# Optimization experiments

Measured on AMD Instinct MI355X. Metric: run time of the kernel, lower is better.

The kernel has to match this reference:

```python
import jax, jax.numpy as jnp
import numpy as np

B, N, IN, H, I, A, NA, NH = 4096, 8, 256, 256, 64, 64, 32, 256
VAR_FLOOR = 0.002
BN_EPS = 1e-5


def _lin(x, w, b):
    # torch Linear: x @ w.T + b, w: [out, in]
    return x @ w.T + b


def _bn_train(x, g, b):
    # BatchNorm1d in training mode: batch stats, biased variance
    mu = jnp.mean(x, axis=0)
    var = jnp.var(x, axis=0)
    return (x - mu) * jax.lax.rsqrt(var + BN_EPS) * g + b


def _intent_net(h_la, w1, b1, g, bbn, w2, b2):
    z = _lin(h_la, w1, b1)
    z = _bn_train(z, g, bbn)
    z = jax.nn.leaky_relu(z, 0.01)
    return _lin(z, w2, b2)


def setup_inputs() -> dict:
    key = jax.random.key(0)
    ks = jax.random.split(key, 30)
    s = 0.05
    d = {
        "inputs": jax.random.normal(ks[0], (B * N, IN), jnp.float32),
        "last_actions": jax.random.normal(ks[1], (B, N, NA), jnp.float32),
        "hidden_state": jax.random.normal(ks[2], (B * N, H), jnp.float32),
        "eps": jax.random.normal(ks[3], (B * N, I), jnp.float32),
        # fc1
        "fc1_w": jax.random.normal(ks[4], (H, IN), jnp.float32) * s,
        "fc1_b": jnp.zeros((H,), jnp.float32),
        # GRUCell (r,z,n gate order, torch layout)
        "gru_w_ih": jax.random.normal(ks[5], (3 * H, H), jnp.float32) * s,
        "gru_w_hh": jax.random.normal(ks[6], (3 * H, H), jnp.float32) * s,
        "gru_b_ih": jnp.zeros((3 * H,), jnp.float32),
        "gru_b_hh": jnp.zeros((3 * H,), jnp.float32),
        # intent_net: Linear(H+NA, NH) -> BN -> LeakyReLU -> Linear(NH, 2*I)
        "in1_w": jax.random.normal(ks[7], (NH, H + NA), jnp.float32) * s,
        "in1_b": jnp.zeros((NH,), jnp.float32),
        "bn_g": jnp.ones((NH,), jnp.float32),
        "bn_b": jnp.zeros((NH,), jnp.float32),
        "in2_w": jax.random.normal(ks[8], (2 * I, NH), jnp.float32) * s,
        "in2_b": jnp.zeros((2 * I,), jnp.float32),
        # attention projections
        "wq_w": jax.random.normal(ks[9], (A, I), jnp.float32) * s,
        "wq_b": jnp.zeros((A,), jnp.float32),
        "wk_w": jax.random.normal(ks[10], (A, I), jnp.float32) * s,
        "wk_b": jnp.zeros((A,), jnp.float32),
        "wv_w": jax.random.normal(ks[11], (A, I + H), jnp.float32) * s,
        "wv_b": jnp.zeros((A,), jnp.float32),
        # fc2
        "fc2_w": jax.random.normal(ks[12], (NA, H + A), jnp.float32) * s,
        "fc2_b": jnp.zeros((NA,), jnp.float32),
        "bs": B,
        "t": 1,
    }
    return d


def reference(inputs, last_actions, hidden_state, eps,
              fc1_w, fc1_b, gru_w_ih, gru_w_hh, gru_b_ih, gru_b_hh,
              in1_w, in1_b, bn_g, bn_b, in2_w, in2_b,
              wq_w, wq_b, wk_w, wk_b, wv_w, wv_b, fc2_w, fc2_b,
              bs, t):
    n = N
    x = jax.nn.relu(_lin(inputs, fc1_w, fc1_b))  # [bs*n, H]
    h_in = hidden_state.reshape(-1, H)
    # torch GRUCell
    gi = x @ gru_w_ih.T + gru_b_ih
    gh = h_in @ gru_w_hh.T + gru_b_hh
    i_r, i_z, i_n = jnp.split(gi, 3, axis=-1)
    h_r, h_z, h_n = jnp.split(gh, 3, axis=-1)
    r = jax.nn.sigmoid(i_r + h_r)
    z = jax.nn.sigmoid(i_z + h_z)
    nng = jnp.tanh(i_n + r * h_n)
    h = (1.0 - z) * nng + z * h_in  # [bs*n, H]

    la = last_actions.reshape(bs * n, NA)
    h_la = jnp.concatenate([h, la], axis=-1)
    ip = _intent_net(h_la, in1_w, in1_b, bn_g, bn_b, in2_w, in2_b)  # [bs*n, 2I]
    mean = ip[:, :I]
    std = jnp.maximum(jnp.exp(ip[:, I:]), VAR_FLOOR)
    intent = mean + eps * std  # reparameterized sample, [bs*n, I]

    q = _lin(intent, wq_w, wq_b).reshape(bs, n, A)  # query per agent i
    k = _lin(intent, wk_w, wk_b).reshape(bs, n, A)  # key per agent j
    scale = 1.0 / jnp.sqrt(jnp.float32(A))
    alpha = jnp.einsum('bia,bja->bij', q * scale, k)  # [bs, n, n]
    diag = jnp.eye(n, dtype=bool)
    alpha = jnp.where(diag[None], -1e9, alpha)
    alpha = jax.nn.softmax(alpha, axis=-1)

    v = _lin(jnp.concatenate([intent, h], axis=-1), wv_w, wv_b).reshape(bs, n, A)
    combined = jnp.einsum('bij,bja->bia', alpha, v).reshape(bs * n, A)

    local_Q = _lin(jnp.concatenate([h, combined], axis=-1), fc2_w, fc2_b).reshape(bs, n, NA)
    # final intent_embed: fresh intent_net output (no clamp/exp applied)
    intent_embed = _intent_net(h_la, in1_w, in1_b, bn_g, bn_b, in2_w, in2_b)
    return local_Q, h, intent, intent_embed
```

## Files before the change

### kernel.cpp

```cpp
#include <hip/hip_runtime.h>
#include <hip/hip_bf16.h>

#define BN_ 32768

using bf16 = __hip_bfloat16;
typedef __bf16 v8bf __attribute__((ext_vector_type(8)));
typedef unsigned short v8us __attribute__((ext_vector_type(8)));
typedef float v4f __attribute__((ext_vector_type(4)));

__device__ __forceinline__ float b2f(bf16 x) { return __bfloat162float(x); }
__device__ __forceinline__ bf16 f2b(float x) { return __float2bfloat16(x); }
__device__ __forceinline__ unsigned short f2bu(float x) {
  bf16 h = __float2bfloat16(x);
  return *reinterpret_cast<unsigned short*>(&h);
}
__device__ __forceinline__ float bu2f(unsigned short u) {
  union { unsigned int i; float f; } x;
  x.i = ((unsigned int)u) << 16;
  return x.f;
}
__device__ __forceinline__ void gl_lds16(const void* g, void* l) {
  __builtin_amdgcn_global_load_lds(
      (const __attribute__((address_space(1))) void*)g,
      (__attribute__((address_space(3))) void*)l, 16, 0, 0);
}
__device__ __forceinline__ float fsig(float x) { return 1.f / (1.f + __expf(-x)); }
__device__ __forceinline__ float ftanh(float x) {
  return 1.f - 2.f / (__expf(2.f * x) + 1.f);
}
template <int CF>
__device__ __forceinline__ void cstore(void* C, size_t off, float v) {
  if constexpr (CF) ((float*)C)[off] = v;
  else ((bf16*)C)[off] = f2b(v);
}
__device__ __forceinline__ int xcd_swz() {
  const int nbx = gridDim.x, nby = gridDim.y;
  const int f = blockIdx.y * nbx + blockIdx.x;
  const int nwg = nbx * nby;
  const int q = nwg >> 3, r = nwg & 7;
  const int xcd = f & 7, l = f >> 3;
  if (r == 0) return xcd * q + l;
  return (xcd < r ? xcd * (q + 1) : r * (q + 1) + (xcd - r) * q) + l;
}

template <int TM, int TN, int WR, int WC, int ACT, int A1M, int A2M, int KS, int KSB,
          int CF>
__global__ __launch_bounds__(256) void gemm_bt(
    const void* __restrict__ A1, int lda1, const void* __restrict__ A2, int lda2,
    const bf16* __restrict__ B1, const bf16* __restrict__ B2, int ldb,
    const float* __restrict__ bias, void* C, int ldc, int K) {
  constexpr int BK = 64;
  __shared__ __align__(16) unsigned short As[TM * BK];
  __shared__ __align__(16) unsigned short Bs[TN * BK];
  const int tid = threadIdx.x;
  const int wv = tid >> 6;
  const int lane = tid & 63;
  const int w = xcd_swz();
  const int bm = (w / gridDim.y) * TM;
  const int bn = (w % gridDim.y) * TN;

  constexpr int WM = TM / WR, WN = TN / WC;
  constexpr int FM = WM / 16, FN = WN / 16;
  const int wm0 = (wv % WR) * WM;
  const int wn0 = (wv / WR) * WN;

  v4f acc[FM][FN];
  const v4f vzero = {0.f, 0.f, 0.f, 0.f};
  for (int i = 0; i < FM; ++i)
    for (int j = 0; j < FN; ++j) acc[i][j] = vzero;

  const int lrow = lane >> 3;
  const int lcol = (lane & 7) * 8;
  const int mr = lane & 15;
  const int kq = (lane >> 4) * 8;

  for (int k0 = 0; k0 < K; k0 += BK) {
    {
      const bool useA1 = (KS == 0) || (k0 < KS);
      const void* Ap = useA1 ? A1 : A2;
      const int lda = useA1 ? lda1 : lda2;
      const int ka = useA1 ? k0 : k0 - KS;
      const bool f32 = useA1 ? (A1M == 1) : (A2M == 1);
      if (f32) {
        const float* Af = (const float*)Ap;
        for (int ch = wv; ch < TM / 8; ch += 4) {
          const float* s = Af + (size_t)(bm + ch * 8 + lrow) * lda + ka + lcol;
          float4 x0 = *(const float4*)s;
          float4 x1 = *(const float4*)(s + 4);
          v8us d;
          d[0]=f2bu(x0.x); d[1]=f2bu(x0.y); d[2]=f2bu(x0.z); d[3]=f2bu(x0.w);
          d[4]=f2bu(x1.x); d[5]=f2bu(x1.y); d[6]=f2bu(x1.z); d[7]=f2bu(x1.w);
          *(v8us*)(As + ch * 8 * BK + lane * 8) = d;
        }
      } else {
        const unsigned short* Ab = (const unsigned short*)Ap;
        for (int ch = wv; ch < TM / 8; ch += 4)
          gl_lds16(Ab + (size_t)(bm + ch * 8 + lrow) * lda + ka + lcol,
                   As + ch * 8 * BK);
      }
    }
    {
      const bool useB1 = (KSB == 0) || (k0 < KSB);
      const bf16* Bp = useB1 ? B1 : B2;
      const int kb = useB1 ? k0 : k0 - KSB;
      for (int ch = wv; ch < TN / 8; ch += 4)
        gl_lds16((const unsigned short*)Bp + (size_t)(bn + ch * 8 + lrow) * ldb + kb + lcol,
                 Bs + ch * 8 * BK);
    }
    __syncthreads();
#pragma unroll
    for (int kk = 0; kk < BK; kk += 32) {
      v8bf af[FM], bfr[FN];
#pragma unroll
      for (int i = 0; i < FM; ++i)
        af[i] = *(const v8bf*)(As + (wm0 + i * 16 + mr) * BK + kk + kq);
#pragma unroll
      for (int j = 0; j < FN; ++j)
        bfr[j] = *(const v8bf*)(Bs + (wn0 + j * 16 + mr) * BK + kk + kq);
#pragma unroll
      for (int i = 0; i < FM; ++i)
#pragma unroll
        for (int j = 0; j < FN; ++j)
          acc[i][j] = __builtin_amdgcn_mfma_f32_16x16x32_bf16(af[i], bfr[j],
                                                              acc[i][j], 0, 0, 0);
    }
    __syncthreads();
  }
  const int crow = (lane >> 4) * 4;
#pragma unroll
  for (int j = 0; j < FN; ++j) {
    const int gcol = bn + wn0 + j * 16 + mr;
    const float bv = bias[gcol];
#pragma unroll
    for (int i = 0; i < FM; ++i) {
#pragma unroll
      for (int r = 0; r < 4; ++r) {
        const int grow = bm + wm0 + i * 16 + crow + r;
        size_t off = (size_t)grow * ldc + gcol;
        float v = acc[i][j][r] + bv;
        if (ACT == 1) v = v > 0.f ? v : 0.f;
        cstore<CF>(C, off, v);
      }
    }
  }
}

__global__ __launch_bounds__(256) void gru_fused(
    const bf16* __restrict__ X, const bf16* __restrict__ HB,
    const bf16* __restrict__ Win, const bf16* __restrict__ Whn,
    const float* __restrict__ FBp, const bf16* __restrict__ G1,
    float* __restrict__ Hout) {
  constexpr int BK = 64;
  __shared__ __align__(16) char smem[69632];
  unsigned short* AsX = (unsigned short*)smem;
  unsigned short* AsH = AsX + 8192;
  unsigned short* Bin = AsH + 8192;
  unsigned short* Bhn = Bin + 8192;
  float* Ein = (float*)smem;
  float* Ehn = (float*)(smem + 34816);

  const int tid = threadIdx.x;
  const int wv = tid >> 6;
  const int lane = tid & 63;
  const int w = xcd_swz();
  const int bm = (w / gridDim.y) * 128;
  const int bn = (w % gridDim.y) * 128;
  const int wm0 = (wv & 1) * 64;
  const int wn0 = (wv >> 1) * 64;

  v4f ain[4][4], ahn[4][4];
  const v4f vzero = {0.f, 0.f, 0.f, 0.f};
  for (int i = 0; i < 4; ++i)
    for (int j = 0; j < 4; ++j) { ain[i][j] = vzero; ahn[i][j] = vzero; }

  const int lrow = lane >> 3;
  const int lcol = (lane & 7) * 8;
  const int mr = lane & 15;
  const int kq = (lane >> 4) * 8;

  for (int k0 = 0; k0 < 256; k0 += BK) {
    for (int ch = wv; ch < 16; ch += 4) {
      const size_t aoff = (size_t)(bm + ch * 8 + lrow) * 256 + k0 + lcol;
      gl_lds16((const unsigned short*)X + aoff, AsX + ch * 8 * BK);
      gl_lds16((const unsigned short*)HB + aoff, AsH + ch * 8 * BK);
      const size_t boff = (size_t)(bn + ch * 8 + lrow) * 256 + k0 + lcol;
      gl_lds16((const unsigned short*)Win + boff, Bin + ch * 8 * BK);
      gl_lds16((const unsigned short*)Whn + boff, Bhn + ch * 8 * BK);
    }
    __syncthreads();
#pragma unroll
    for (int kk = 0; kk < BK; kk += 32) {
      v8bf ax[4], ah[4], bi[4], bh[4];
#pragma unroll
      for (int i = 0; i < 4; ++i) {
        ax[i] = *(const v8bf*)(AsX + (wm0 + i * 16 + mr) * BK + kk + kq);
        ah[i] = *(const v8bf*)(AsH + (wm0 + i * 16 + mr) * BK + kk + kq);
      }
#pragma unroll
      for (int j = 0; j < 4; ++j) {
        bi[j] = *(const v8bf*)(Bin + (wn0 + j * 16 + mr) * BK + kk + kq);
        bh[j] = *(const v8bf*)(Bhn + (wn0 + j * 16 + mr) * BK + kk + kq);
      }
#pragma unroll
      for (int i = 0; i < 4; ++i)
#pragma unroll
        for (int j = 0; j < 4; ++j) {
          ain[i][j] = __builtin_amdgcn_mfma_f32_16x16x32_bf16(ax[i], bi[j],
                                                              ain[i][j], 0, 0, 0);
          ahn[i][j] = __builtin_amdgcn_mfma_f32_16x16x32_bf16(ah[i], bh[j],
                                                              ahn[i][j], 0, 0, 0);
        }
    }
    __syncthreads();
  }

  const int crow = (lane >> 4) * 4;
  const int myhalf = wn0 >> 6;
  const int c4 = (tid & 15) * 4;
#pragma unroll
  for (int h = 0; h < 2; ++h) {
    __syncthreads();
    if (myhalf == h) {
#pragma unroll
      for (int i = 0; i < 4; ++i)
#pragma unroll
        for (int j = 0; j < 4; ++j)
#pragma unroll
          for (int r = 0; r < 4; ++r) {
            const int idx = (wm0 + i * 16 + crow + r) * 68 + j * 16 + mr;
            Ein[idx] = ain[i][j][r];
            Ehn[idx] = ahn[i][j][r];
          }
    }
    __syncthreads();
#pragma unroll
    for (int it = 0; it < 8; ++it) {
      const int row = (tid >> 4) + it * 16;
      const int grow = bm + row;
      const int gcol = bn + h * 64 + c4;
      const unsigned short* g1p = (const unsigned short*)G1 + (size_t)grow * 512 + gcol;
      const ushort4 r4 = *(const ushort4*)g1p;
      const ushort4 z4 = *(const ushort4*)(g1p + 256);
      const ushort4 hp4 = *(const ushort4*)((const unsigned short*)HB +
                                            (size_t)grow * 256 + gcol);
      const float4 ei = *(const float4*)(Ein + row * 68 + c4);
      const float4 eh = *(const float4*)(Ehn + row * 68 + c4);
      const float4 bin4 = *(const float4*)(FBp + 768 + gcol);
      const float4 bhn4 = *(const float4*)(FBp + 1024 + gcol);
      const float rv[4] = {bu2f(r4.x), bu2f(r4.y), bu2f(r4.z), bu2f(r4.w)};
      const float zv[4] = {bu2f(z4.x), bu2f(z4.y), bu2f(z4.z), bu2f(z4.w)};
      const float hpv[4] = {bu2f(hp4.x), bu2f(hp4.y), bu2f(hp4.z), bu2f(hp4.w)};
      const float eiv[4] = {ei.x, ei.y, ei.z, ei.w};
      const float ehv[4] = {eh.x, eh.y, eh.z, eh.w};
      const float biv[4] = {bin4.x, bin4.y, bin4.z, bin4.w};
      const float bhv[4] = {bhn4.x, bhn4.y, bhn4.z, bhn4.w};
      float vo[4];
#pragma unroll
      for (int u = 0; u < 4; ++u) {
        float rr = fsig(rv[u]);
        float zz = fsig(zv[u]);
        float nn = ftanh(eiv[u] + biv[u] + rr * (ehv[u] + bhv[u]));
        vo[u] = (1.f - zz) * nn + zz * hpv[u];
      }
      *(float4*)(Hout + (size_t)grow * 256 + gcol) =
          make_float4(vo[0], vo[1], vo[2], vo[3]);
    }
  }
}

__global__ void conv_all(
    const float* fc1_w, const float* w_ih, const float* w_hh, const float* in1_w,
    const float* in2_w, const float* wq_w, const float* wk_w, const float* wv_w,
    const float* fc2_w, const float* fc1_b, const float* b_ih, const float* b_hh,
    const float* in1_b, const float* in2_b, const float* wq_b, const float* wk_b,
    const float* wv_b, const float* fc2_b, const float* bn_g, const float* bn_b,
    bf16* __restrict__ WF, float* __restrict__ FB) {
  int idx = blockIdx.x * 256 + threadIdx.x;
  if (idx < 612352) {
    float v;
    if (idx < 65536) v = fc1_w[idx];
    else if (idx < 262144) v = w_ih[idx - 65536];
    else if (idx < 458752) v = w_hh[idx - 262144];
    else if (idx < 540672) {
      int j = idx - 458752, r = j / 320, c = j % 320;
      v = (c < 288) ? in1_w[r * 288 + c] : 0.f;
    } else if (idx < 573440) v = in2_w[idx - 540672];
    else if (idx < 581632) {
      int j = idx - 573440, r = j >> 6, c = j & 63;
      v = (r < 64) ? wq_w[r * 64 + c] : wk_w[(r - 64) * 64 + c];
    } else if (idx < 602112) v = wv_w[idx - 581632];
    else v = fc2_w[idx - 602112];
    WF[idx] = f2b(v);
  } else if (idx < 615936) {
    int j = idx - 612352;
    float v;
    if (j < 256) v = fc1_b[j];
    else if (j < 768) v = b_ih[j - 256] + b_hh[j - 256];
    else if (j < 1024) v = b_ih[512 + j - 768];
    else if (j < 1280) v = b_hh[512 + j - 1024];
    else if (j < 1536) v = in1_b[j - 1280];
    else if (j < 1664) v = in2_b[j - 1536];
    else if (j < 1792) { int c = j - 1664; v = (c < 64) ? wq_b[c] : wk_b[c - 64]; }
    else if (j < 1856) v = wv_b[j - 1792];
    else if (j < 1888) v = fc2_b[j - 1856];
    else if (j < 2144) v = bn_g[j - 1888];
    else if (j < 2400) v = bn_b[j - 2144];
    else v = 0.f;
    FB[j] = v;
  }
}

__global__ void f2b_copy(const float* __restrict__ s, bf16* __restrict__ d) {
  int i = blockIdx.x * 256 + threadIdx.x;
  const float4 a = ((const float4*)s)[i * 2];
  const float4 b = ((const float4*)s)[i * 2 + 1];
  v8us o;
  o[0]=f2bu(a.x); o[1]=f2bu(a.y); o[2]=f2bu(a.z); o[3]=f2bu(a.w);
  o[4]=f2bu(b.x); o[5]=f2bu(b.y); o[6]=f2bu(b.z); o[7]=f2bu(b.w);
  ((v8us*)d)[i] = o;
}

__global__ void pack_la(const float* __restrict__ la, bf16* __restrict__ lap) {
  int idx = blockIdx.x * 256 + threadIdx.x;
  int row = idx >> 6, c = idx & 63;
  lap[idx] = f2b((c < 32) ? la[(size_t)row * 32 + c] : 0.f);
}

__global__ void bn_reduce(const bf16* __restrict__ Z1, float* __restrict__ stats) {
  int col = threadIdx.x;
  float s = 0.f, q = 0.f;
  for (int r = blockIdx.x; r < BN_; r += 256) {
    float v = b2f(Z1[(size_t)r * 256 + col]);
    s += v; q += v * v;
  }
  atomicAdd(&stats[col], s);
  atomicAdd(&stats[256 + col], q);
}

__global__ void bn_finalize(const float* __restrict__ g, const float* __restrict__ b,
                            float* __restrict__ stats) {
  int c = threadIdx.x;
  float mean = stats[c] * (1.f / 32768.f);
  float var = stats[256 + c] * (1.f / 32768.f) - mean * mean;
  var = fmaxf(var, 0.f);
  float sc = g[c] * rsqrtf(var + 1e-5f);
  stats[512 + c] = sc;
  stats[768 + c] = b[c] - mean * sc;
}

__global__ void bn_leaky(const bf16* __restrict__ Z1, const float* __restrict__ stats,
                         bf16* __restrict__ zt) {
  int idx = blockIdx.x * 256 + threadIdx.x;
  int col = idx & 255;
  float v = b2f(Z1[idx]) * stats[512 + col] + stats[768 + col];
  zt[idx] = f2b(v > 0.f ? v : 0.01f * v);
}

__global__ void make_intent(const float* __restrict__ ie, const float* __restrict__ eps,
                            float* __restrict__ intent) {
  int idx = blockIdx.x * 256 + threadIdx.x;
  int row = idx >> 6, c = idx & 63;
  float mean = ie[(size_t)row * 128 + c];
  float sd = fmaxf(expf(ie[(size_t)row * 128 + 64 + c]), 0.002f);
  intent[idx] = mean + eps[idx] * sd;
}

__global__ __launch_bounds__(64) void attn(const bf16* __restrict__ QK,
                                           const bf16* __restrict__ Vv,
                                           bf16* __restrict__ comb) {
  __shared__ float q[8][65], k[8][65], v[8][65];
  __shared__ float al[8][8];
  int b = blockIdx.x, t = threadIdx.x;
  size_t rb = (size_t)b * 8;
  for (int u = 0; u < 8; ++u) {
    q[u][t] = b2f(QK[(rb + u) * 128 + t]);
    k[u][t] = b2f(QK[(rb + u) * 128 + 64 + t]);
    v[u][t] = b2f(Vv[(rb + u) * 64 + t]);
  }
  __syncthreads();
  int i = t >> 3, j = t & 7;
  float s = 0.f;
#pragma unroll
  for (int a = 0; a < 64; ++a) s += q[i][a] * k[j][a];
  s *= 0.125f;
  if (i == j) s = -1e9f;
  float m = s;
  m = fmaxf(m, __shfl_xor(m, 1, 8));
  m = fmaxf(m, __shfl_xor(m, 2, 8));
  m = fmaxf(m, __shfl_xor(m, 4, 8));
  float e = expf(s - m);
  float sum = e;
  sum += __shfl_xor(sum, 1, 8);
  sum += __shfl_xor(sum, 2, 8);
  sum += __shfl_xor(sum, 4, 8);
  al[i][j] = e / sum;
  __syncthreads();
  int a0 = (t & 7) * 8;
  for (int u = 0; u < 8; ++u) {
    float o = 0.f;
#pragma unroll
    for (int jj = 0; jj < 8; ++jj) o += al[i][jj] * v[jj][a0 + u];
    comb[(rb + i) * 64 + a0 + u] = f2b(o);
  }
}

extern "C" void kernel_launch(void* const* d_in, const int* in_sizes, int n_in,
                              void* d_out, int out_size, void* d_ws, size_t ws_size,
                              hipStream_t stream) {
  (void)in_sizes; (void)n_in; (void)out_size; (void)ws_size;
  const float* inputs = (const float*)d_in[0];
  const float* last_actions = (const float*)d_in[1];
  const float* hidden = (const float*)d_in[2];
  const float* eps = (const float*)d_in[3];

  float* out = (float*)d_out;
  float* out_lq = out;
  float* out_h = out + 1048576;
  float* out_it = out + 9437184;
  float* out_ie = out + 11534336;

  bf16* HB = (bf16*)(out + 11534336);

  char* ws = (char*)d_ws;
  bf16* X    = (bf16*)(ws + 0);
  bf16* G1   = (bf16*)(ws + 16777216);
  bf16* LAP  = (bf16*)(ws + 16777216);
  bf16* ZT   = (bf16*)(ws + 20971520);
  bf16* Z1   = (bf16*)(ws + 0);
  bf16* QK   = (bf16*)(ws + 0);
  bf16* V    = (bf16*)(ws + 8388608);
  bf16* COMB = (bf16*)(ws + 12582912);
  float* FB  = (float*)(ws + 50331648);
  bf16*  WF  = (bf16*)(ws + 50348032);
  float* stats = FB + 2560;

  conv_all<<<2406, 256, 0, stream>>>(
      (const float*)d_in[4], (const float*)d_in[6], (const float*)d_in[7],
      (const float*)d_in[10], (const float*)d_in[14], (const float*)d_in[16],
      (const float*)d_in[18], (const float*)d_in[20], (const float*)d_in[22],
      (const float*)d_in[5], (const float*)d_in[8], (const float*)d_in[9],
      (const float*)d_in[11], (const float*)d_in[15], (const float*)d_in[17],
      (const float*)d_in[19], (const float*)d_in[21], (const float*)d_in[23],
      (const float*)d_in[12], (const float*)d_in[13], WF, FB);

  f2b_copy<<<4096, 256, 0, stream>>>(hidden, HB);

  gemm_bt<128, 128, 2, 2, 1, 1, 0, 0, 0, 0><<<dim3(256, 2), 256, 0, stream>>>(
      inputs, 256, nullptr, 0, WF + 0, nullptr, 256, FB + 0, X, 256, 256);
  gemm_bt<128, 128, 2, 2, 0, 0, 0, 256, 256, 0><<<dim3(256, 4), 256, 0, stream>>>(
      X, 256, HB, 256, WF + 65536, WF + 262144, 256, FB + 256, G1, 512, 512);
  gru_fused<<<dim3(256, 2), 256, 0, stream>>>(
      X, HB, WF + 65536 + 512 * 256, WF + 262144 + 512 * 256, FB, G1, out_h);

  pack_la<<<8192, 256, 0, stream>>>(last_actions, LAP);
  gemm_bt<128, 128, 2, 2, 0, 1, 0, 256, 0, 0><<<dim3(256, 2), 256, 0, stream>>>(
      out_h, 256, LAP, 64, WF + 458752, nullptr, 320, FB + 1280, Z1, 256, 320);
  bn_reduce<<<256, 256, 0, stream>>>(Z1, stats);
  bn_finalize<<<1, 256, 0, stream>>>(FB + 1888, FB + 2144, stats);
  bn_leaky<<<32768, 256, 0, stream>>>(Z1, stats, ZT);
  gemm_bt<128, 128, 2, 2, 0, 0, 0, 0, 0, 1><<<dim3(256, 1), 256, 0, stream>>>(
      ZT, 256, nullptr, 0, WF + 540672, nullptr, 256, FB + 1536, out_ie, 128, 256);
  make_intent<<<8192, 256, 0, stream>>>(out_ie, eps, out_it);
  gemm_bt<128, 128, 2, 2, 0, 1, 0, 0, 0, 0><<<dim3(256, 1), 256, 0, stream>>>(
      out_it, 64, nullptr, 0, WF + 573440, nullptr, 64, FB + 1664, QK, 128, 64);
  gemm_bt<128, 64, 4, 1, 0, 1, 1, 64, 0, 0><<<dim3(256, 1), 256, 0, stream>>>(
      out_it, 64, out_h, 256, WF + 581632, nullptr, 320, FB + 1792, V, 64, 320);
  attn<<<4096, 64, 0, stream>>>(QK, V, COMB);
  gemm_bt<128, 32, 4, 1, 0, 1, 0, 256, 0, 1><<<dim3(256, 1), 256, 0, stream>>>(
      out_h, 256, COMB, 64, WF + 602112, nullptr, 320, FB + 1856, out_lq, 32, 320);
}
```

Measured before the change: 373.6 us.

## Fuse BN-apply into GEMM A-load, emit bf16 h/intent copies, vectorize BN and attention

The BN scale/shift and LeakyReLU are folded into the A-tile load of the second intent GEMM, which removes the separate bn_leaky pass and the ZT buffer. The GRU and make_intent kernels now also write bf16 copies of h and intent into a shared strided buffer, so later GEMMs read bf16 through the async LDS path instead of converting fp32 on every load. bn_reduce is vectorized with shared-memory partial reduction, and attn packs four batches per 256-thread block with vector loads and stores. LAP is moved into the output local_Q region, and the shared buffers are aliased in the workspace, which adds more extra writes and more aliasing risk.

After: 396.8 us. 1.06x slower.

```diff
diff --git a/kernel.cpp b/kernel.cpp
--- a/kernel.cpp
+++ b/kernel.cpp
@@ -44,11 +44,12 @@
 }
 
 template <int TM, int TN, int WR, int WC, int ACT, int A1M, int A2M, int KS, int KSB,
-          int CF>
+          int CF, int ATF>
 __global__ __launch_bounds__(256) void gemm_bt(
     const void* __restrict__ A1, int lda1, const void* __restrict__ A2, int lda2,
     const bf16* __restrict__ B1, const bf16* __restrict__ B2, int ldb,
-    const float* __restrict__ bias, void* C, int ldc, int K) {
+    const float* __restrict__ bias, void* C, int ldc, int K,
+    const float* __restrict__ tsc, const float* __restrict__ tsh) {
   constexpr int BK = 64;
   __shared__ __align__(16) unsigned short As[TM * BK];
   __shared__ __align__(16) unsigned short Bs[TN * BK];
@@ -81,7 +82,26 @@
       const int lda = useA1 ? lda1 : lda2;
       const int ka = useA1 ? k0 : k0 - KS;
       const bool f32 = useA1 ? (A1M == 1) : (A2M == 1);
-      if (f32) {
+      if (ATF && useA1) {
+        const unsigned short* Ab = (const unsigned short*)Ap;
+        const float4 s0 = *(const float4*)(tsc + ka + lcol);
+        const float4 s1 = *(const float4*)(tsc + ka + lcol + 4);
+        const float4 h0 = *(const float4*)(tsh + ka + lcol);
+        const float4 h1 = *(const float4*)(tsh + ka + lcol + 4);
+        const float sc[8] = {s0.x, s0.y, s0.z, s0.w, s1.x, s1.y, s1.z, s1.w};
+        const float sh[8] = {h0.x, h0.y, h0.z, h0.w, h1.x, h1.y, h1.z, h1.w};
+        for (int ch = wv; ch < TM / 8; ch += 4) {
+          const unsigned short* s = Ab + (size_t)(bm + ch * 8 + lrow) * lda + ka + lcol;
+          v8us zin = *(const v8us*)s;
+          v8us d;
+#pragma unroll
+          for (int u = 0; u < 8; ++u) {
+            float v = bu2f(zin[u]) * sc[u] + sh[u];
+            d[u] = f2bu(v > 0.f ? v : 0.01f * v);
+          }
+          *(v8us*)(As + ch * 8 * BK + lane * 8) = d;
+        }
+      } else if (f32) {
         const float* Af = (const float*)Ap;
         for (int ch = wv; ch < TM / 8; ch += 4) {
           const float* s = Af + (size_t)(bm + ch * 8 + lrow) * lda + ka + lcol;
@@ -148,7 +168,7 @@
 __global__ __launch_bounds__(256) void gru_fused(
     const bf16* __restrict__ X, const bf16* __restrict__ HB,
     const bf16* __restrict__ Win, const bf16* __restrict__ Whn,
-    const float* __restrict__ FBp, const bf16* __restrict__ G1,
+    const float* __restrict__ FBp, const bf16* G1, unsigned short* HB2,
     float* __restrict__ Hout) {
   constexpr int BK = 64;
   __shared__ __align__(16) char smem[69632];
@@ -264,6 +284,10 @@
       }
       *(float4*)(Hout + (size_t)grow * 256 + gcol) =
           make_float4(vo[0], vo[1], vo[2], vo[3]);
+      ushort4 hb2;
+      hb2.x = f2bu(vo[0]); hb2.y = f2bu(vo[1]);
+      hb2.z = f2bu(vo[2]); hb2.w = f2bu(vo[3]);
+      *(ushort4*)(HB2 + (size_t)grow * 512 + gcol) = hb2;
     }
   }
 }
@@ -326,15 +350,47 @@
   lap[idx] = f2b((c < 32) ? la[(size_t)row * 32 + c] : 0.f);
 }
 
-__global__ void bn_reduce(const bf16* __restrict__ Z1, float* __restrict__ stats) {
-  int col = threadIdx.x;
-  float s = 0.f, q = 0.f;
-  for (int r = blockIdx.x; r < BN_; r += 256) {
-    float v = b2f(Z1[(size_t)r * 256 + col]);
-    s += v; q += v * v;
-  }
-  atomicAdd(&stats[col], s);
-  atomicAdd(&stats[256 + col], q);
+__global__ __launch_bounds__(256) void bn_reduce(const bf16* __restrict__ Z1,
+                                                 float* __restrict__ stats) {
+  const int cg = threadIdx.x & 31;
+  const int rl = threadIdx.x >> 5;
+  float s[8], q[8];
+#pragma unroll
+  for (int u = 0; u < 8; ++u) { s[u] = 0.f; q[u] = 0.f; }
+  for (int r = blockIdx.x * 8 + rl; r < BN_; r += 2048) {
+    v8us z = *(const v8us*)((const unsigned short*)Z1 + (size_t)r * 256 + cg * 8);
+#pragma unroll
+    for (int u = 0; u < 8; ++u) {
+      float v = bu2f(z[u]);
+      s[u] += v; q[u] += v * v;
+    }
+  }
+  __shared__ float red[2048];
+#pragma unroll
+  for (int u = 0; u < 8; ++u) red[rl * 256 + cg * 8 + u] = s[u];
+  __syncthreads();
+  if (rl == 0) {
+#pragma unroll
+    for (int u = 0; u < 8; ++u) {
+      float t = 0.f;
+#pragma unroll
+      for (int k = 0; k < 8; ++k) t += red[k * 256 + cg * 8 + u];
+      atomicAdd(&stats[cg * 8 + u], t);
+    }
+  }
+  __syncthreads();
+#pragma unroll
+  for (int u = 0; u < 8; ++u) red[rl * 256 + cg * 8 + u] = q[u];
+  __syncthreads();
+  if (rl == 0) {
+#pragma unroll
+    for (int u = 0; u < 8; ++u) {
+      float t = 0.f;
+#pragma unroll
+      for (int k = 0; k < 8; ++k) t += red[k * 256 + cg * 8 + u];
+      atomicAdd(&stats[256 + cg * 8 + u], t);
+    }
+  }
 }
 
 __global__ void bn_finalize(const float* __restrict__ g, const float* __restrict__ b,
@@ -348,60 +404,74 @@
   stats[768 + c] = b[c] - mean * sc;
 }
 
-__global__ void bn_leaky(const bf16* __restrict__ Z1, const float* __restrict__ stats,
-                         bf16* __restrict__ zt) {
-  int idx = blockIdx.x * 256 + threadIdx.x;
-  int col = idx & 255;
-  float v = b2f(Z1[idx]) * stats[512 + col] + stats[768 + col];
-  zt[idx] = f2b(v > 0.f ? v : 0.01f * v);
-}
-
 __global__ void make_intent(const float* __restrict__ ie, const float* __restrict__ eps,
-                            float* __restrict__ intent) {
+                            float* __restrict__ intent, unsigned short* __restrict__ itb) {
   int idx = blockIdx.x * 256 + threadIdx.x;
   int row = idx >> 6, c = idx & 63;
   float mean = ie[(size_t)row * 128 + c];
   float sd = fmaxf(expf(ie[(size_t)row * 128 + 64 + c]), 0.002f);
-  intent[idx] = mean + eps[idx] * sd;
-}
-
-__global__ __launch_bounds__(64) void attn(const bf16* __restrict__ QK,
-                                           const bf16* __restrict__ Vv,
-                                           bf16* __restrict__ comb) {
-  __shared__ float q[8][65], k[8][65], v[8][65];
-  __shared__ float al[8][8];
-  int b = blockIdx.x, t = threadIdx.x;
-  size_t rb = (size_t)b * 8;
-  for (int u = 0; u < 8; ++u) {
-    q[u][t] = b2f(QK[(rb + u) * 128 + t]);
-    k[u][t] = b2f(QK[(rb + u) * 128 + 64 + t]);
-    v[u][t] = b2f(Vv[(rb + u) * 64 + t]);
+  float v = mean + eps[idx] * sd;
+  intent[idx] = v;
+  itb[(size_t)row * 512 + c] = f2bu(v);
+}
+
+__global__ __launch_bounds__(256) void attn(const bf16* __restrict__ QK,
+                                            const bf16* __restrict__ Vv,
+                                            bf16* __restrict__ comb) {
+  __shared__ float q[4][8][65], k[4][8][65], v[4][8][65];
+  __shared__ float al[4][8][8];
+  const int wv = threadIdx.x >> 6, t = threadIdx.x & 63;
+  const int b = blockIdx.x * 4 + wv;
+  const size_t rb = (size_t)b * 8;
+  const unsigned short* qkb = (const unsigned short*)QK + rb * 128;
+#pragma unroll
+  for (int p = 0; p < 2; ++p) {
+    const int e = t * 8 + p * 512;
+    const int row = e >> 7, col = e & 127;
+    v8us d = *(const v8us*)(qkb + row * 128 + col);
+    if (col < 64) {
+#pragma unroll
+      for (int u = 0; u < 8; ++u) q[wv][row][col + u] = bu2f(d[u]);
+    } else {
+#pragma unroll
+      for (int u = 0; u < 8; ++u) k[wv][row][col - 64 + u] = bu2f(d[u]);
+    }
+  }
+  {
+    const int e = t * 8;
+    const int row = e >> 6, col = e & 63;
+    v8us d = *(const v8us*)((const unsigned short*)Vv + rb * 64 + row * 64 + col);
+#pragma unroll
+    for (int u = 0; u < 8; ++u) v[wv][row][col + u] = bu2f(d[u]);
   }
   __syncthreads();
-  int i = t >> 3, j = t & 7;
+  const int i = t >> 3, j = t & 7;
   float s = 0.f;
 #pragma unroll
-  for (int a = 0; a < 64; ++a) s += q[i][a] * k[j][a];
+  for (int a = 0; a < 64; ++a) s += q[wv][i][a] * k[wv][j][a];
   s *= 0.125f;
   if (i == j) s = -1e9f;
   float m = s;
   m = fmaxf(m, __shfl_xor(m, 1, 8));
   m = fmaxf(m, __shfl_xor(m, 2, 8));
   m = fmaxf(m, __shfl_xor(m, 4, 8));
-  float e = expf(s - m);
+  float e = __expf(s - m);
   float sum = e;
   sum += __shfl_xor(sum, 1, 8);
   sum += __shfl_xor(sum, 2, 8);
   sum += __shfl_xor(sum, 4, 8);
-  al[i][j] = e / sum;
+  al[wv][i][j] = e / sum;
   __syncthreads();
-  int a0 = (t & 7) * 8;
+  const int a0 = (t & 7) * 8;
+  v8us o8;
+#pragma unroll
   for (int u = 0; u < 8; ++u) {
     float o = 0.f;
 #pragma unroll
-    for (int jj = 0; jj < 8; ++jj) o += al[i][jj] * v[jj][a0 + u];
-    comb[(rb + i) * 64 + a0 + u] = f2b(o);
-  }
+    for (int jj = 0; jj < 8; ++jj) o += al[wv][i][jj] * v[wv][jj][a0 + u];
+    o8[u] = f2bu(o);
+  }
+  *(v8us*)((unsigned short*)comb + (rb + i) * 64 + a0) = o8;
 }
 
 extern "C" void kernel_launch(void* const* d_in, const int* in_sizes, int n_in,
@@ -420,12 +490,13 @@
   float* out_ie = out + 11534336;
 
   bf16* HB = (bf16*)(out + 11534336);
+  bf16* LAP = (bf16*)out_lq;
 
   char* ws = (char*)d_ws;
   bf16* X    = (bf16*)(ws + 0);
   bf16* G1   = (bf16*)(ws + 16777216);
-  bf16* LAP  = (bf16*)(ws + 16777216);
-  bf16* ZT   = (bf16*)(ws + 20971520);
+  unsigned short* HB2 = (unsigned short*)(ws + 16777216);
+  unsigned short* ITB = (unsigned short*)(ws + 16777216) + 256;
   bf16* Z1   = (bf16*)(ws + 0);
   bf16* QK   = (bf16*)(ws + 0);
   bf16* V    = (bf16*)(ws + 8388608);
@@ -444,28 +515,34 @@
       (const float*)d_in[12], (const float*)d_in[13], WF, FB);
 
   f2b_copy<<<4096, 256, 0, stream>>>(hidden, HB);
-
-  gemm_bt<128, 128, 2, 2, 1, 1, 0, 0, 0, 0><<<dim3(256, 2), 256, 0, stream>>>(
-      inputs, 256, nullptr, 0, WF + 0, nullptr, 256, FB + 0, X, 256, 256);
-  gemm_bt<128, 128, 2, 2, 0, 0, 0, 256, 256, 0><<<dim3(256, 4), 256, 0, stream>>>(
-      X, 256, HB, 256, WF + 65536, WF + 262144, 256, FB + 256, G1, 512, 512);
+  pack_la<<<8192, 256, 0, stream>>>(last_actions, LAP);
+
+  gemm_bt<128, 128, 2, 2, 1, 1, 0, 0, 0, 0, 0><<<dim3(256, 2), 256, 0, stream>>>(
+      inputs, 256, nullptr, 0, WF + 0, nullptr, 256, FB + 0, X, 256, 256,
+      nullptr, nullptr);
+  gemm_bt<128, 128, 2, 2, 0, 0, 0, 256, 256, 0, 0><<<dim3(256, 4), 256, 0, stream>>>(
+      X, 256, HB, 256, WF + 65536, WF + 262144, 256, FB + 256, G1, 512, 512,
+      nullptr, nullptr);
   gru_fused<<<dim3(256, 2), 256, 0, stream>>>(
-      X, HB, WF + 65536 + 512 * 256, WF + 262144 + 512 * 256, FB, G1, out_h);
-
-  pack_la<<<8192, 256, 0, stream>>>(last_actions, LAP);
-  gemm_bt<128, 128, 2, 2, 0, 1, 0, 256, 0, 0><<<dim3(256, 2), 256, 0, stream>>>(
-      out_h, 256, LAP, 64, WF + 458752, nullptr, 320, FB + 1280, Z1, 256, 320);
+      X, HB, WF + 65536 + 512 * 256, WF + 262144 + 512 * 256, FB, G1, HB2, out_h);
+
+  gemm_bt<128, 128, 2, 2, 0, 0, 0, 256, 0, 0, 0><<<dim3(256, 2), 256, 0, stream>>>(
+      HB2, 512, LAP, 64, WF + 458752, nullptr, 320, FB + 1280, Z1, 256, 320,
+      nullptr, nullptr);
   bn_reduce<<<256, 256, 0, stream>>>(Z1, stats);
   bn_finalize<<<1, 256, 0, stream>>>(FB + 1888, FB + 2144, stats);
-  bn_leaky<<<32768, 256, 0, stream>>>(Z1, stats, ZT);
-  gemm_bt<128, 128, 2, 2, 0, 0, 0, 0, 0, 1><<<dim3(256, 1), 256, 0, stream>>>(
-      ZT, 256, nullptr, 0, WF + 540672, nullptr, 256, FB + 1536, out_ie, 128, 256);
-  make_intent<<<8192, 256, 0, stream>>>(out_ie, eps, out_it);
-  gemm_bt<128, 128, 2, 2, 0, 1, 0, 0, 0, 0><<<dim3(256, 1), 256, 0, stream>>>(
-      out_it, 64, nullptr, 0, WF + 573440, nullptr, 64, FB + 1664, QK, 128, 64);
-  gemm_bt<128, 64, 4, 1, 0, 1, 1, 64, 0, 0><<<dim3(256, 1), 256, 0, stream>>>(
-      out_it, 64, out_h, 256, WF + 581632, nullptr, 320, FB + 1792, V, 64, 320);
-  attn<<<4096, 64, 0, stream>>>(QK, V, COMB);
-  gemm_bt<128, 32, 4, 1, 0, 1, 0, 256, 0, 1><<<dim3(256, 1), 256, 0, stream>>>(
-      out_h, 256, COMB, 64, WF + 602112, nullptr, 320, FB + 1856, out_lq, 32, 320);
-}
+  gemm_bt<128, 128, 2, 2, 0, 0, 0, 0, 0, 1, 1><<<dim3(256, 1), 256, 0, stream>>>(
+      Z1, 256, nullptr, 0, WF + 540672, nullptr, 256, FB + 1536, out_ie, 128, 256,
+      stats + 512, stats + 768);
+  make_intent<<<8192, 256, 0, stream>>>(out_ie, eps, out_it, ITB);
+  gemm_bt<128, 128, 2, 2, 0, 0, 0, 0, 0, 0, 0><<<dim3(256, 1), 256, 0, stream>>>(
+      ITB, 512, nullptr, 0, WF + 573440, nullptr, 64, FB + 1664, QK, 128, 64,
+      nullptr, nullptr);
+  gemm_bt<128, 64, 4, 1, 0, 0, 0, 64, 0, 0, 0><<<dim3(256, 1), 256, 0, stream>>>(
+      ITB, 512, HB2, 512, WF + 581632, nullptr, 320, FB + 1792, V, 64, 320,
+      nullptr, nullptr);
+  attn<<<1024, 256, 0, stream>>>(QK, V, COMB);
+  gemm_bt<128, 32, 4, 1, 0, 0, 0, 256, 0, 1, 0><<<dim3(256, 1), 256, 0, stream>>>(
+      HB2, 512, COMB, 64, WF + 602112, nullptr, 320, FB + 1856, out_lq, 32, 320,
+      nullptr, nullptr);
+}
```
